# Optimization experiments

Hardware: AMD Instinct MI355X
Metric: run time of the kernel (lower is better)

Reference implementation:

```python
import jax, jax.numpy as jnp
import numpy as np

NT, NV, ND, NM, NP = 50000, 1000, 20000, 5000, 8000
E = 100000
D, H, C = 256, 4, 64          # gnn_hidden_dim, heads, per-head channels
TS_FEAT, EMB, L = 64, 128, 2
NEG_SLOPE = 0.2

SIZES = {'ts': NT, 'vital': NV, 'diag': ND, 'med': NM, 'proc': NP}
EDGE_TYPES = [('ts', 'vital'), ('vital', 'ts'), ('ts', 'diag'), ('diag', 'ts'),
              ('ts', 'med'), ('med', 'ts'), ('ts', 'proc'), ('proc', 'ts')]
T = len(EDGE_TYPES)


def setup_inputs():
    key = jax.random.key(0)
    ks = jax.random.split(key, 32)
    def nrm(k, shape, s=0.05):
        return jax.random.normal(k, shape, dtype=jnp.float32) * s
    inp = {}
    inp['ts_x'] = nrm(ks[0], (NT, TS_FEAT), 1.0)
    inp['emb_vital'] = nrm(ks[1], (NV, EMB), 1.0)
    inp['emb_diag'] = nrm(ks[2], (ND, EMB), 1.0)
    inp['emb_med'] = nrm(ks[3], (NM, EMB), 1.0)
    inp['emb_proc'] = nrm(ks[4], (NP, EMB), 1.0)
    inp['Wp_ts'] = nrm(ks[5], (TS_FEAT, D)); inp['bp_ts'] = jnp.zeros((D,), jnp.float32)
    inp['Wp_c'] = nrm(ks[6], (4, EMB, D)); inp['bp_c'] = jnp.zeros((4, D), jnp.float32)
    inp['Wsrc'] = nrm(ks[7], (L, T, D, H * C))
    inp['Wdst'] = nrm(ks[8], (L, T, D, H * C))
    inp['asrc'] = nrm(ks[9], (L, T, H, C))
    inp['adst'] = nrm(ks[10], (L, T, H, C))
    inp['bconv'] = jnp.zeros((L, T, H * C), jnp.float32)
    inp['Wc1'] = nrm(ks[11], (D, D // 2)); inp['bc1'] = jnp.zeros((D // 2,), jnp.float32)
    inp['Wc2'] = nrm(ks[12], (D // 2, 1)); inp['bc2'] = jnp.zeros((1,), jnp.float32)
    names = ['ei_tv', 'ei_vt', 'ei_td', 'ei_dt', 'ei_tm', 'ei_mt', 'ei_tp', 'ei_pt']
    for i, ((s, d), nm) in enumerate(zip(EDGE_TYPES, names)):
        k1, k2 = jax.random.split(ks[13 + i])
        src = jax.random.randint(k1, (E,), 0, SIZES[s], dtype=jnp.int32)
        dst = jax.random.randint(k2, (E,), 0, SIZES[d], dtype=jnp.int32)
        inp[nm] = jnp.stack([src, dst])
    return inp


def gat_conv(xs, xd, Ws, Wd, a_s, a_d, b, ei, nd):
    """Bipartite PyG GATConv: add_self_loops=False, concat heads, eval (no dropout)."""
    hs = (xs @ Ws).reshape(-1, H, C)            # [Ns,H,C]
    hd = (xd @ Wd).reshape(-1, H, C)            # [Nd,H,C]
    es = jnp.sum(hs * a_s, axis=-1)             # [Ns,H]
    ed = jnp.sum(hd * a_d, axis=-1)             # [Nd,H]
    src, dst = ei[0], ei[1]
    e = jax.nn.leaky_relu(es[src] + ed[dst], NEG_SLOPE)   # [E,H]
    m = jax.ops.segment_max(e, dst, num_segments=nd)      # segment softmax over dst
    ex = jnp.exp(e - m[dst])
    den = jax.ops.segment_sum(ex, dst, num_segments=nd)
    alpha = ex / (den[dst] + 1e-16)
    msg = (alpha[:, :, None] * hs[src]).reshape(-1, H * C)  # [E,H*C]
    return jax.ops.segment_sum(msg, dst, num_segments=nd) + b


def _forward(ts_x, emb_vital, emb_diag, emb_med, emb_proc, Wp_ts, bp_ts, Wp_c, bp_c,
             Wsrc, Wdst, asrc, adst, bconv, Wc1, bc1, Wc2, bc2, edges):
    x = {'ts': ts_x @ Wp_ts + bp_ts,
         'vital': emb_vital @ Wp_c[0] + bp_c[0],
         'diag': emb_diag @ Wp_c[1] + bp_c[1],
         'med': emb_med @ Wp_c[2] + bp_c[2],
         'proc': emb_proc @ Wp_c[3] + bp_c[3]}
    for l in range(L):
        new = {k: jnp.zeros((SIZES[k], D), jnp.float32) for k in x}  # HeteroConv aggr='sum'
        for t, ((s, d), ei) in enumerate(zip(EDGE_TYPES, edges)):
            new[d] = new[d] + gat_conv(x[s], x[d], Wsrc[l, t], Wdst[l, t],
                                       asrc[l, t], adst[l, t], bconv[l, t], ei, SIZES[d])
        x = {k: jax.nn.relu(v) for k, v in new.items()}
    g = jnp.mean(x['ts'], axis=0)               # graph embedding
    h = jax.nn.relu(g @ Wc1 + bc1)
    logits = h @ Wc2 + bc2
    return jnp.squeeze(logits, -1)              # output_classes == 1 -> scalar


def reference(ts_x, emb_vital, emb_diag, emb_med, emb_proc, Wp_ts, bp_ts, Wp_c, bp_c,
              Wsrc, Wdst, asrc, adst, bconv, Wc1, bc1, Wc2, bc2,
              ei_tv, ei_vt, ei_td, ei_dt, ei_tm, ei_mt, ei_tp, ei_pt):
    edges = (ei_tv, ei_vt, ei_td, ei_dt, ei_tm, ei_mt, ei_tp, ei_pt)
    return _forward(ts_x, emb_vital, emb_diag, emb_med, emb_proc, Wp_ts, bp_ts, Wp_c, bp_c,
                    Wsrc, Wdst, asrc, adst, bconv, Wc1, bc1, Wc2, bc2, edges)
```

## Files before the change

### kernel.cpp

```cpp
#include <hip/hip_runtime.h>

#define E_N 100000
#define NDST 234000

typedef __attribute__((ext_vector_type(8))) short bfrag8;
typedef __attribute__((ext_vector_type(4))) float accf4;

__device__ __forceinline__ void atomAddF(float* p, float v) { unsafeAtomicAdd(p, v); }
__device__ __forceinline__ float lrelu(float v) { return v >= 0.f ? v : 0.2f * v; }

__device__ __forceinline__ unsigned short f2bf(float f) {
    unsigned u = __float_as_uint(f);
    return (unsigned short)((u + 0x7FFFu + ((u >> 16) & 1u)) >> 16);
}
__device__ __forceinline__ float bf2f(unsigned short h) {
    return __uint_as_float(((unsigned)h) << 16);
}

__constant__ int c_tbase[8] = {0, 1000, 51000, 71000, 121000, 126000, 176000, 184000};
__constant__ int c_co4[4]   = {0, 1000, 21000, 26000};

struct EI8 { const int* p[8]; };

struct BTJob { const float* W; unsigned short* hi; unsigned short* lo; int K; int kshift; };
struct BTBatch { BTJob j[17]; };

struct MJob { const float* A; const unsigned short* BThi; const unsigned short* BTlo;
              float* C; unsigned short* Cbf; const float* bias; int M; int K; int relu; };
struct MBatch { MJob j[8]; };

__device__ __forceinline__ void gemm_body(const MJob jb, int bx)
{
    const int rowblk = (bx >> 4) * 8 + (bx & 7);
    const int half = (bx >> 3) & 1;
    const int bm = rowblk * 128;
    if (bm >= jb.M) return;
    const int bn = half * 128;
    const int M = jb.M, K = jb.K;

    __shared__ unsigned short Ah[128 * 40];
    __shared__ unsigned short Al[128 * 40];
    __shared__ unsigned short B1[128 * 40];
    __shared__ unsigned short B2[128 * 40];

    const int tid  = threadIdx.x;
    const int wv   = tid >> 6;
    const int lane = tid & 63;
    const int qr = wv >> 1, qc = wv & 1;
    const int lm = lane & 15;
    const int lq = lane >> 4;

    accf4 acc[4][4] = {};

    for (int k0 = 0; k0 < K; k0 += 32) {
#pragma unroll
        for (int it = 0; it < 4; ++it) {
            int slot = it * 256 + tid;
            int m  = slot >> 3;
            int kq = (slot & 7) << 2;
            float4 v = make_float4(0.f, 0.f, 0.f, 0.f);
            if (bm + m < M) v = *(const float4*)(jb.A + (size_t)(bm + m) * K + k0 + kq);
            int o = m * 40 + kq;
            unsigned short h0 = f2bf(v.x), h1 = f2bf(v.y), h2 = f2bf(v.z), h3 = f2bf(v.w);
            Ah[o + 0] = h0; Ah[o + 1] = h1; Ah[o + 2] = h2; Ah[o + 3] = h3;
            Al[o + 0] = f2bf(v.x - bf2f(h0));
            Al[o + 1] = f2bf(v.y - bf2f(h1));
            Al[o + 2] = f2bf(v.z - bf2f(h2));
            Al[o + 3] = f2bf(v.w - bf2f(h3));
        }
#pragma unroll
        for (int it = 0; it < 2; ++it) {
            int slot = it * 256 + tid;
            int n  = slot >> 2;
            int kq = (slot & 3) << 3;
            size_t go = (size_t)(bn + n) * K + k0 + kq;
            *(uint4*)&B1[n * 40 + kq] = *(const uint4*)(jb.BThi + go);
            *(uint4*)&B2[n * 40 + kq] = *(const uint4*)(jb.BTlo + go);
        }
        __syncthreads();

        bfrag8 ah[4], al[4], b1[4], b2[4];
#pragma unroll
        for (int t = 0; t < 4; ++t) {
            int am  = qr * 64 + t * 16 + lm;
            int bnn = qc * 64 + t * 16 + lm;
            ah[t] = *(const bfrag8*)&Ah[am * 40 + lq * 8];
            al[t] = *(const bfrag8*)&Al[am * 40 + lq * 8];
            b1[t] = *(const bfrag8*)&B1[bnn * 40 + lq * 8];
            b2[t] = *(const bfrag8*)&B2[bnn * 40 + lq * 8];
        }
#pragma unroll
        for (int mt = 0; mt < 4; ++mt)
#pragma unroll
            for (int nt = 0; nt < 4; ++nt) {
                acc[mt][nt] = __builtin_amdgcn_mfma_f32_16x16x32_bf16(ah[mt], b1[nt], acc[mt][nt], 0, 0, 0);
                acc[mt][nt] = __builtin_amdgcn_mfma_f32_16x16x32_bf16(al[mt], b1[nt], acc[mt][nt], 0, 0, 0);
                acc[mt][nt] = __builtin_amdgcn_mfma_f32_16x16x32_bf16(ah[mt], b2[nt], acc[mt][nt], 0, 0, 0);
            }
        __syncthreads();
    }

#pragma unroll
    for (int nt = 0; nt < 4; ++nt) {
        int col = bn + qc * 64 + nt * 16 + lm;
        float bv = jb.bias ? jb.bias[col] : 0.f;
#pragma unroll
        for (int mt = 0; mt < 4; ++mt) {
            int row0 = bm + qr * 64 + mt * 16 + lq * 4;
#pragma unroll
            for (int r = 0; r < 4; ++r) {
                int row = row0 + r;
                if (row < M) {
                    float o = acc[mt][nt][r] + bv;
                    if (jb.relu) o = fmaxf(o, 0.f);
                    if (jb.C)   jb.C[(size_t)row * 256 + col] = o;
                    if (jb.Cbf) jb.Cbf[(size_t)row * 256 + col] = f2bf(o);
                }
            }
        }
    }
}

struct Prep1 { BTBatch bt; const float* Wsrc; const float* Wdst; const float* asrc;
               const float* adst; float* weff; EI8 ei; int* cnt; };

__global__ __launch_bounds__(256) void prep1_k(Prep1 a)
{
    int bx = blockIdx.x;
    if (bx < 4352) {
        BTJob jb = a.bt.j[bx >> 8];
        int idx = (bx & 255) * 256 + threadIdx.x;
        if (idx >= (jb.K << 8)) return;
        int n = idx >> jb.kshift;
        int k = idx & (jb.K - 1);
        float w = jb.W[(size_t)k * 256 + n];
        unsigned short h = f2bf(w);
        jb.hi[idx] = h;
        jb.lo[idx] = f2bf(w - bf2f(h));
    } else if (bx < 4672) {
        int idx = (bx - 4352) * 256 + threadIdx.x;
        if (idx >= 81920) return;
        int col = idx & 31;
        int k   = (idx >> 5) & 255;
        int lnt = idx >> 13;
        int nt  = lnt % 5;
        int l   = lnt / 5;
        bool is_src; int t, h;
        if (nt == 0) {
            if (col < 16) { is_src = true;  t = (col >> 2) * 2;            h = col & 3; }
            else          { is_src = false; t = ((col - 16) >> 2) * 2 + 1; h = col & 3; }
        } else {
            if (col < 4)      { is_src = true;  t = 2 * nt - 1; h = col; }
            else if (col < 8) { is_src = false; t = 2 * nt - 2; h = col - 4; }
            else { a.weff[idx] = 0.f; return; }
        }
        const float* W = (is_src ? a.Wsrc : a.Wdst) + ((size_t)((l * 8 + t) * 256 + k)) * 256 + h * 64;
        const float* av = (is_src ? a.asrc : a.adst) + ((size_t)((l * 8 + t) * 4 + h)) * 64;
        float val = 0.f;
        for (int c = 0; c < 64; c++) val += W[c] * av[c];
        a.weff[idx] = val;
    } else {
        int g = (bx - 4672) * 256 + threadIdx.x;
        if (g >= 8 * E_N) return;
        int t = g / E_N;
        int i = g - t * E_N;
        int d = a.ei.p[t][E_N + i];
        atomicAdd(&a.cnt[c_tbase[t] + d], 1);
    }
}

__global__ __launch_bounds__(256) void prep2_k(const float* __restrict__ Wp_ts,
                                               const float* __restrict__ bp_ts,
                                               const float* __restrict__ Wp_c,
                                               const float* __restrict__ bp_c,
                                               const float* __restrict__ weff,
                                               float* __restrict__ effT, float* __restrict__ biasT,
                                               float* __restrict__ effC, float* __restrict__ biasC,
                                               const int* __restrict__ cnt,
                                               int* __restrict__ rowptr, int* __restrict__ bsum)
{
    if (blockIdx.x < 25) {
        int idx = blockIdx.x * 256 + threadIdx.x;
        if (idx < 2048) {
            int kk = idx >> 5, j = idx & 31;
            float s = 0.f;
            for (int k = 0; k < 256; k++) s += Wp_ts[kk * 256 + k] * weff[k * 32 + j];
            effT[idx] = s;
        } else if (idx < 2080) {
            int j = idx - 2048;
            float s = 0.f;
            for (int k = 0; k < 256; k++) s += bp_ts[k] * weff[k * 32 + j];
            biasT[j] = s;
        } else if (idx < 2080 + 4 * 1032) {
            int r = idx - 2080;
            int q = r / 1032; r -= q * 1032;
            const float* wq = weff + (q + 1) * 8192;
            if (r < 1024) {
                int kk = r >> 3, j = r & 7;
                float s = 0.f;
                for (int k = 0; k < 256; k++) s += Wp_c[(size_t)q * 32768 + kk * 256 + k] * wq[k * 32 + j];
                effC[(q * 128 + kk) * 8 + j] = s;
            } else {
                int j = r - 1024;
                float s = 0.f;
                for (int k = 0; k < 256; k++) s += bp_c[q * 256 + k] * wq[k * 32 + j];
                biasC[q * 8 + j] = s;
            }
        }
    } else {
        __shared__ int sd[256];
        int b = blockIdx.x - 25, t = threadIdx.x;
        int base = b * 1024 + t * 4;
        int v0 = 0, v1 = 0, v2 = 0, v3 = 0;
        if (base + 0 < NDST) v0 = cnt[base + 0];
        if (base + 1 < NDST) v1 = cnt[base + 1];
        if (base + 2 < NDST) v2 = cnt[base + 2];
        if (base + 3 < NDST) v3 = cnt[base + 3];
        int s = v0 + v1 + v2 + v3;
        sd[t] = s;
        __syncthreads();
        for (int off = 1; off < 256; off <<= 1) {
            int x = 0;
            if (t >= off) x = sd[t - off];
            __syncthreads();
            if (t >= off) sd[t] += x;
            __syncthreads();
        }
        int run = sd[t] - s;
        if (t == 255) bsum[b] = sd[255];
        if (base + 0 < NDST) rowptr[base + 0] = run;          run += v0;
        if (base + 1 < NDST) rowptr[base + 1] = run;          run += v1;
        if (base + 2 < NDST) rowptr[base + 2] = run;          run += v2;
        if (base + 3 < NDST) rowptr[base + 3] = run;
    }
}

__global__ __launch_bounds__(256) void scanB(int* __restrict__ bsum, int nb)
{
    __shared__ int sd[256];
    int t = threadIdx.x;
    int v = (t < nb) ? bsum[t] : 0;
    sd[t] = v;
    __syncthreads();
    for (int off = 1; off < 256; off <<= 1) {
        int x = 0;
        if (t >= off) x = sd[t - off];
        __syncthreads();
        if (t >= off) sd[t] += x;
        __syncthreads();
    }
    if (t < nb) bsum[t] = sd[t] - v;
}

struct Prep3 { int* rowptr; const int* bsum; int* cursor;
               const float* ts_x; const float* effT; const float* biasT; float* attnT;
               const float* e0; const float* e1; const float* e2; const float* e3;
               const float* effC; const float* biasC; float* attnC; };

__global__ __launch_bounds__(256) void prep3_k(Prep3 a)
{
    int bx = blockIdx.x;
    if (bx < 229) {
        int t = threadIdx.x;
        int off = a.bsum[bx];
        int base = bx * 1024 + t * 4;
#pragma unroll
        for (int j = 0; j < 4; j++) {
            int i = base + j;
            if (i < NDST) {
                int r = a.rowptr[i] + off;
                a.rowptr[i] = r;
                a.cursor[i] = r;
            }
        }
        if (bx == 0 && t == 0) a.rowptr[NDST] = 8 * E_N;
    } else if (bx < 425) {
        int n = (bx - 229) * 256 + threadIdx.x;
        if (n >= 50000) return;
        float acc[32];
#pragma unroll
        for (int j = 0; j < 32; j++) acc[j] = a.biasT[j];
        const float* xr = a.ts_x + (size_t)n * 64;
        for (int k = 0; k < 64; k += 4) {
            float4 xv = *(const float4*)(xr + k);
#pragma unroll
            for (int j = 0; j < 32; j++)
                acc[j] += xv.x * a.effT[(k + 0) * 32 + j] + xv.y * a.effT[(k + 1) * 32 + j]
                        + xv.z * a.effT[(k + 2) * 32 + j] + xv.w * a.effT[(k + 3) * 32 + j];
        }
#pragma unroll
        for (int j = 0; j < 32; j++) a.attnT[(size_t)n * 32 + j] = acc[j];
    } else {
        int m = (bx - 425) * 256 + threadIdx.x;
        if (m >= 34000) return;
        int q, loc;
        if (m < 1000)       { q = 0; loc = m; }
        else if (m < 21000) { q = 1; loc = m - 1000; }
        else if (m < 26000) { q = 2; loc = m - 21000; }
        else                { q = 3; loc = m - 26000; }
        const float* er = (q == 0 ? a.e0 : q == 1 ? a.e1 : q == 2 ? a.e2 : a.e3) + (size_t)loc * 128;
        const float* W = a.effC + q * 1024;
        float acc[8];
#pragma unroll
        for (int j = 0; j < 8; j++) acc[j] = a.biasC[q * 8 + j];
        for (int k = 0; k < 128; k += 4) {
            float4 xv = *(const float4*)(er + k);
#pragma unroll
            for (int j = 0; j < 8; j++)
                acc[j] += xv.x * W[(k + 0) * 8 + j] + xv.y * W[(k + 1) * 8 + j]
                        + xv.z * W[(k + 2) * 8 + j] + xv.w * W[(k + 3) * 8 + j];
        }
#pragma unroll
        for (int j = 0; j < 8; j++) a.attnC[(size_t)m * 8 + j] = acc[j];
    }
}

struct ProjPlace { MBatch mb; EI8 ei; int* cursor; int* ssrc; int* sdst; float* exf;
                   const float* attnT; const float* attnC; };

__global__ __launch_bounds__(256, 2) void projplace_k(ProjPlace a)
{
    if (blockIdx.x < 3920) {
        gemm_body(a.mb.j[blockIdx.x / 784], blockIdx.x % 784);
    } else {
        int g = (blockIdx.x - 3920) * 256 + threadIdx.x;
        if (g >= 8 * E_N) return;
        int t = g / E_N;
        int i = g - t * E_N;
        int d = a.ei.p[t][E_N + i];
        int s = a.ei.p[t][i];
        int pos = atomicAdd(&a.cursor[c_tbase[t] + d], 1);
        a.ssrc[pos] = s;
        a.sdst[pos] = d;
        int q = t >> 1;
        float4 ex;
        if ((t & 1) == 0) {
            int w = c_co4[q] + d;
            int soff = 4 * q;
            ex.x = __expf(lrelu(a.attnT[(size_t)s * 32 + soff + 0] + a.attnC[(size_t)w * 8 + 4]));
            ex.y = __expf(lrelu(a.attnT[(size_t)s * 32 + soff + 1] + a.attnC[(size_t)w * 8 + 5]));
            ex.z = __expf(lrelu(a.attnT[(size_t)s * 32 + soff + 2] + a.attnC[(size_t)w * 8 + 6]));
            ex.w = __expf(lrelu(a.attnT[(size_t)s * 32 + soff + 3] + a.attnC[(size_t)w * 8 + 7]));
        } else {
            int m = c_co4[q] + s;
            int doff = 16 + 4 * q;
            ex.x = __expf(lrelu(a.attnC[(size_t)m * 8 + 0] + a.attnT[(size_t)d * 32 + doff + 0]));
            ex.y = __expf(lrelu(a.attnC[(size_t)m * 8 + 1] + a.attnT[(size_t)d * 32 + doff + 1]));
            ex.z = __expf(lrelu(a.attnC[(size_t)m * 8 + 2] + a.attnT[(size_t)d * 32 + doff + 2]));
            ex.w = __expf(lrelu(a.attnC[(size_t)m * 8 + 3] + a.attnT[(size_t)d * 32 + doff + 3]));
        }
        *(float4*)(a.exf + (size_t)pos * 4) = ex;
    }
}

__device__ __forceinline__ float4 agg_core(const float* __restrict__ exf,
                                           const unsigned short* __restrict__ hscbf,
                                           const int* __restrict__ rowptr,
                                           const int* __restrict__ ssrc,
                                           const float* __restrict__ bconv_l,
                                           int d, int h, int ch)
{
    const int co4[4] = {0, 1000, 21000, 26000};
    const int tb4[4] = {1000, 71000, 126000, 184000};
    const int bo4[4] = {256, 768, 1280, 1792};
    float ax = 0.f, ay = 0.f, az = 0.f, aw = 0.f;
#pragma unroll
    for (int q = 0; q < 4; q++) {
        int r0 = rowptr[tb4[q] + d], r1 = rowptr[tb4[q] + d + 1];
        float den = 0.f, sx = 0.f, sy = 0.f, sz = 0.f, sw = 0.f;
        int e = r0;
        for (; e + 2 <= r1; e += 2) {
            int sA = ssrc[e], sB = ssrc[e + 1];
            float xA = exf[(size_t)e * 4 + h];
            float xB = exf[(size_t)(e + 1) * 4 + h];
            ushort4 rA = *(const ushort4*)(hscbf + (size_t)(co4[q] + sA) * 256 + ch);
            ushort4 rB = *(const ushort4*)(hscbf + (size_t)(co4[q] + sB) * 256 + ch);
            den += xA + xB;
            sx += xA * bf2f(rA.x) + xB * bf2f(rB.x);
            sy += xA * bf2f(rA.y) + xB * bf2f(rB.y);
            sz += xA * bf2f(rA.z) + xB * bf2f(rB.z);
            sw += xA * bf2f(rA.w) + xB * bf2f(rB.w);
        }
        if (e < r1) {
            int s = ssrc[e];
            float x = exf[(size_t)e * 4 + h];
            den += x;
            ushort4 hv = *(const ushort4*)(hscbf + (size_t)(co4[q] + s) * 256 + ch);
            sx += x * bf2f(hv.x); sy += x * bf2f(hv.y);
            sz += x * bf2f(hv.z); sw += x * bf2f(hv.w);
        }
        const float* b = bconv_l + bo4[q] + ch;
        float inv = 1.f / (den + 1e-16f);
        ax += b[0] + sx * inv; ay += b[1] + sy * inv;
        az += b[2] + sz * inv; aw += b[3] + sw * inv;
    }
    float4 o;
    o.x = fmaxf(ax, 0.f); o.y = fmaxf(ay, 0.f);
    o.z = fmaxf(az, 0.f); o.w = fmaxf(aw, 0.f);
    return o;
}

struct L1A { MBatch mb; const float* exf; const unsigned short* xtsbf;
             const int* rowptr; const int* ssrc; float* aggx; };

__global__ __launch_bounds__(256, 2) void l1a_k(L1A a)
{
    if (blockIdx.x < 1280) {
        gemm_body(a.mb.j[blockIdx.x / 320], blockIdx.x % 320);
        return;
    }
    int w = (blockIdx.x - 1280) * 4 + (threadIdx.x >> 6);
    int lane = threadIdx.x & 63;
    int h = lane >> 4;
    int ch = (h << 6) | ((lane & 15) << 2);
    int q, dloc;
    if (w < 1000)       { q = 0; dloc = w; }
    else if (w < 21000) { q = 1; dloc = w - 1000; }
    else if (w < 26000) { q = 2; dloc = w - 21000; }
    else                { q = 3; dloc = w - 26000; }
    const int csr4[4] = {0, 51000, 121000, 176000};
    int r0 = a.rowptr[csr4[q] + dloc], r1 = a.rowptr[csr4[q] + dloc + 1];
    float den = 0.f, sx = 0.f, sy = 0.f, sz = 0.f, sw = 0.f;
    int e = r0;
    for (; e + 4 <= r1; e += 4) {
        int sA = a.ssrc[e], sB = a.ssrc[e + 1], sC = a.ssrc[e + 2], sD = a.ssrc[e + 3];
        float xA = a.exf[(size_t)e * 4 + h];
        float xB = a.exf[(size_t)(e + 1) * 4 + h];
        float xC = a.exf[(size_t)(e + 2) * 4 + h];
        float xD = a.exf[(size_t)(e + 3) * 4 + h];
        ushort4 rA = *(const ushort4*)(a.xtsbf + (size_t)sA * 256 + ch);
        ushort4 rB = *(const ushort4*)(a.xtsbf + (size_t)sB * 256 + ch);
        ushort4 rC = *(const ushort4*)(a.xtsbf + (size_t)sC * 256 + ch);
        ushort4 rD = *(const ushort4*)(a.xtsbf + (size_t)sD * 256 + ch);
        den += (xA + xB) + (xC + xD);
        sx += xA * bf2f(rA.x) + xB * bf2f(rB.x) + xC * bf2f(rC.x) + xD * bf2f(rD.x);
        sy += xA * bf2f(rA.y) + xB * bf2f(rB.y) + xC * bf2f(rC.y) + xD * bf2f(rD.y);
        sz += xA * bf2f(rA.z) + xB * bf2f(rB.z) + xC * bf2f(rC.z) + xD * bf2f(rD.z);
        sw += xA * bf2f(rA.w) + xB * bf2f(rB.w) + xC * bf2f(rC.w) + xD * bf2f(rD.w);
    }
    for (; e < r1; e++) {
        int s = a.ssrc[e];
        float x = a.exf[(size_t)e * 4 + h];
        den += x;
        ushort4 rv = *(const ushort4*)(a.xtsbf + (size_t)s * 256 + ch);
        sx += x * bf2f(rv.x); sy += x * bf2f(rv.y);
        sz += x * bf2f(rv.z); sw += x * bf2f(rv.w);
    }
    float inv = 1.f / (den + 1e-16f);
    float4 o; o.x = sx * inv; o.y = sy * inv; o.z = sz * inv; o.w = sw * inv;
    *(float4*)(a.aggx + (size_t)w * 256 + ch) = o;
}

struct L1B { MBatch mb; float* attnT; const float* exf; const unsigned short* hscbf;
             const int* rowptr; const int* ssrc; const float* bconv_l; const float* weff2; };

__global__ __launch_bounds__(256, 2) void l1b_k(L1B a)
{
    if (blockIdx.x < 1280) {
        gemm_body(a.mb.j[blockIdx.x / 320], blockIdx.x % 320);
        return;
    }
    int bx = blockIdx.x - 1280;
    int wv = threadIdx.x >> 6;
    int d = bx * 4 + wv;
    int lane = threadIdx.x & 63;
    int h = lane >> 4;
    int ch = (h << 6) | ((lane & 15) << 2);
    float4 o = agg_core(a.exf, a.hscbf, a.rowptr, a.ssrc, a.bconv_l, d, h, ch);
    __shared__ float rowbuf[4][256];
    rowbuf[wv][ch + 0] = o.x; rowbuf[wv][ch + 1] = o.y;
    rowbuf[wv][ch + 2] = o.z; rowbuf[wv][ch + 3] = o.w;
    __syncthreads();
    int j = lane & 15, seg = lane >> 4;
    const float* rb = rowbuf[wv] + seg * 64;
    const float* w2 = a.weff2 + (seg * 64) * 32 + 16 + j;
    float s = 0.f;
#pragma unroll 8
    for (int c = 0; c < 64; c++) s += rb[c] * w2[c * 32];
    s += __shfl_xor(s, 16);
    s += __shfl_xor(s, 32);
    if (lane < 16) a.attnT[(size_t)d * 32 + 16 + lane] = s;
}

struct L2A { MBatch mb; const float* x1; const float* weff2; float* attnC; };

__global__ __launch_bounds__(256, 2) void l2a_k(L2A a)
{
    if (blockIdx.x < 1280) {
        gemm_body(a.mb.j[blockIdx.x / 320], blockIdx.x % 320);
        return;
    }
    int m = (blockIdx.x - 1280) * 256 + threadIdx.x;
    if (m >= 34000) return;
    int n = 50000 + m;
    int nt = (n < 51000) ? 1 : (n < 71000) ? 2 : (n < 76000) ? 3 : 4;
    const float* xrow = a.x1 + (size_t)n * 256;
    const float* W = a.weff2 + nt * 8192;
    float acc[8];
#pragma unroll
    for (int j = 0; j < 8; j++) acc[j] = 0.f;
    for (int k = 0; k < 256; k += 4) {
        const float4 xv = *(const float4*)(xrow + k);
#pragma unroll
        for (int j = 0; j < 8; j++)
            acc[j] += xv.x * W[(k + 0) * 32 + j] + xv.y * W[(k + 1) * 32 + j]
                    + xv.z * W[(k + 2) * 32 + j] + xv.w * W[(k + 3) * 32 + j];
    }
#pragma unroll
    for (int j = 0; j < 8; j++) a.attnC[(size_t)m * 8 + j] = acc[j];
}

__global__ __launch_bounds__(256) void bake_k(const int* __restrict__ ssrc,
                                              const int* __restrict__ sdst,
                                              const float* __restrict__ attnC,
                                              const float* __restrict__ attnT,
                                              float* __restrict__ exf)
{
    int i = blockIdx.x * 256 + threadIdx.x;
    if (i >= 400000) return;
    int tq = i / E_N;
    int i2 = i - tq * E_N;
    int e = (2 * tq + 1) * E_N + i2;
    int s = ssrc[e], d = sdst[e];
    int m = c_co4[tq] + s;
    int doff = 16 + 4 * tq;
    float4 ex;
    ex.x = __expf(lrelu(attnC[(size_t)m * 8 + 0] + attnT[(size_t)d * 32 + doff + 0]));
    ex.y = __expf(lrelu(attnC[(size_t)m * 8 + 1] + attnT[(size_t)d * 32 + doff + 1]));
    ex.z = __expf(lrelu(attnC[(size_t)m * 8 + 2] + attnT[(size_t)d * 32 + doff + 2]));
    ex.w = __expf(lrelu(attnC[(size_t)m * 8 + 3] + attnT[(size_t)d * 32 + doff + 3]));
    *(float4*)(exf + (size_t)e * 4) = ex;
}

__global__ __launch_bounds__(256) void pool_k(const float* __restrict__ exf,
                                              const unsigned short* __restrict__ hscbf,
                                              const int* __restrict__ rowptr,
                                              const int* __restrict__ ssrc,
                                              const float* __restrict__ bconv_l,
                                              float* __restrict__ part)
{
    int d = blockIdx.x * 4 + (threadIdx.x >> 6);
    int lane = threadIdx.x & 63;
    int h = lane >> 4;
    int ch = (h << 6) | ((lane & 15) << 2);
    float4 o = agg_core(exf, hscbf, rowptr, ssrc, bconv_l, d, h, ch);
    __shared__ float4 red4[256];
    red4[threadIdx.x] = o;
    __syncthreads();
    if (threadIdx.x < 64) {
        float4 a = red4[threadIdx.x], b = red4[threadIdx.x + 64];
        float4 c = red4[threadIdx.x + 128], dd = red4[threadIdx.x + 192];
        float4 s;
        s.x = (a.x + b.x) + (c.x + dd.x);
        s.y = (a.y + b.y) + (c.y + dd.y);
        s.z = (a.z + b.z) + (c.z + dd.z);
        s.w = (a.w + b.w) + (c.w + dd.w);
        int cch = ((threadIdx.x >> 4) << 6) | ((threadIdx.x & 15) << 2);
        *(float4*)(part + (size_t)blockIdx.x * 256 + cch) = s;
    }
}

__global__ __launch_bounds__(256) void colsum_part(const float* __restrict__ part,
                                                   float* __restrict__ gsum)
{
    int c = threadIdx.x;
    float s = 0.f;
    for (int r = blockIdx.x; r < 12500; r += gridDim.x) s += part[(size_t)r * 256 + c];
    atomAddF(gsum + c, s);
}

__global__ __launch_bounds__(128) void head_k(const float* __restrict__ gsum,
                                              const float* __restrict__ Wc1,
                                              const float* __restrict__ bc1,
                                              const float* __restrict__ Wc2,
                                              const float* __restrict__ bc2,
                                              float* __restrict__ out)
{
    __shared__ float g[256];
    __shared__ float red[128];
    int t = threadIdx.x;
    g[t] = gsum[t] * (1.f / 50000.f);
    g[t + 128] = gsum[t + 128] * (1.f / 50000.f);
    __syncthreads();
    float acc = bc1[t];
    for (int k = 0; k < 256; k++) acc += g[k] * Wc1[k * 128 + t];
    red[t] = fmaxf(acc, 0.f) * Wc2[t];
    __syncthreads();
    for (int sft = 64; sft > 0; sft >>= 1) {
        if (t < sft) red[t] += red[t + sft];
        __syncthreads();
    }
    if (t == 0) out[0] = red[0] + bc2[0];
}

extern "C" void kernel_launch(void* const* d_in, const int* in_sizes, int n_in,
                              void* d_out, int out_size, void* d_ws, size_t ws_size,
                              hipStream_t stream)
{
    const float* ts_x   = (const float*)d_in[0];
    const float* emb[4] = {(const float*)d_in[1], (const float*)d_in[2],
                           (const float*)d_in[3], (const float*)d_in[4]};
    const float* Wp_ts  = (const float*)d_in[5];
    const float* bp_ts  = (const float*)d_in[6];
    const float* Wp_c   = (const float*)d_in[7];
    const float* bp_c   = (const float*)d_in[8];
    const float* Wsrc   = (const float*)d_in[9];
    const float* Wdst   = (const float*)d_in[10];
    const float* asrc   = (const float*)d_in[11];
    const float* adst   = (const float*)d_in[12];
    const float* bconv  = (const float*)d_in[13];
    const float* Wc1    = (const float*)d_in[14];
    const float* bc1    = (const float*)d_in[15];
    const float* Wc2    = (const float*)d_in[16];
    const float* bc2    = (const float*)d_in[17];
    EI8 ei;
    for (int t = 0; t < 8; t++) ei.p[t] = (const int*)d_in[18 + t];

    float* x0    = (float*)d_ws;
    float* x1    = x0    + 21504000;
    float* attnT = x1    + 21504000;
    float* attnC = attnT + 1600000;
    float* weff  = attnC + 272000;
    float* gsum  = weff  + 81920;
    float* effT  = gsum  + 256;
    float* biasT = effT  + 2048;
    float* effC  = biasT + 32;
    float* biasC = effC  + 4096;
    int* rowptr  = (int*)(biasC + 32);
    int* bsum    = rowptr + 234004;
    int* ssrc    = bsum + 256;
    unsigned short* xtsbf = (unsigned short*)(ssrc + 800000);
    unsigned short* hscbf = xtsbf + 12800000;
    unsigned short* btp   = hscbf + 8704000;
    int* cursor  = (int*)hscbf;
    float* aggx  = x1;
    float* exf   = x0;
    int* sdst    = (int*)(x0 + 3200000);
    float* part  = x0 + 4200000;

    unsigned short* bt_ts_h = btp;
    unsigned short* bt_ts_l = bt_ts_h + 16384;
    unsigned short* bt_c_h[4], *bt_c_l[4];
    {
        unsigned short* p = bt_ts_l + 16384;
        for (int q = 0; q < 4; q++) { bt_c_h[q] = p; p += 32768; bt_c_l[q] = p; p += 32768; }
    }
    unsigned short* bt_w = bt_ts_l + 16384 + 8 * 32768;
    auto wpan_h = [&](int l, int t) { return bt_w + (size_t)((l == 0 ? t : 8 + t / 2) * 2) * 65536; };
    auto wpan_l = [&](int l, int t) { return wpan_h(l, t) + 65536; };

    static const int Nd4[4]    = {1000, 20000, 5000, 8000};
    static const int co4[4]    = {0, 1000, 21000, 26000};
    static const int dbase4[4] = {50000, 51000, 71000, 76000};
    static const int tsrc[4]   = {1, 3, 5, 7};
    static const int tdst[4]   = {0, 2, 4, 6};

    hipMemsetAsync(cursor, 0, NDST * sizeof(int), stream);

    {
        Prep1 a = {};
        int zi = 0;
        a.bt.j[zi++] = {Wp_ts, bt_ts_h, bt_ts_l, 64, 6};
        for (int q = 0; q < 4; q++)
            a.bt.j[zi++] = {Wp_c + q * 32768, bt_c_h[q], bt_c_l[q], 128, 7};
        for (int t = 0; t < 8; t++)
            a.bt.j[zi++] = {Wsrc + (size_t)(0 * 8 + t) * 65536, wpan_h(0, t), wpan_l(0, t), 256, 8};
        for (int t = 1; t < 8; t += 2)
            a.bt.j[zi++] = {Wsrc + (size_t)(1 * 8 + t) * 65536, wpan_h(1, t), wpan_l(1, t), 256, 8};
        a.Wsrc = Wsrc; a.Wdst = Wdst; a.asrc = asrc; a.adst = adst;
        a.weff = weff; a.ei = ei; a.cnt = cursor;
        prep1_k<<<7797, 256, 0, stream>>>(a);
    }

    prep2_k<<<254, 256, 0, stream>>>(Wp_ts, bp_ts, Wp_c, bp_c, weff,
                                     effT, biasT, effC, biasC, cursor, rowptr, bsum);
    scanB<<<1, 256, 0, stream>>>(bsum, 229);

    {
        Prep3 a = {rowptr, bsum, cursor, ts_x, effT, biasT, attnT,
                   emb[0], emb[1], emb[2], emb[3], effC, biasC, attnC};
        prep3_k<<<558, 256, 0, stream>>>(a);
    }

    {
        ProjPlace a = {};
        a.mb.j[0] = {ts_x, bt_ts_h, bt_ts_l, nullptr, xtsbf, bp_ts, 50000, 64, 0};
        for (int q = 0; q < 4; q++)
            a.mb.j[1 + q] = {emb[q], bt_c_h[q], bt_c_l[q], x0 + (size_t)dbase4[q] * 256,
                             nullptr, bp_c + q * 256, Nd4[q], 128, 0};
        a.ei = ei; a.cursor = cursor; a.ssrc = ssrc; a.sdst = sdst; a.exf = exf;
        a.attnT = attnT; a.attnC = attnC;
        projplace_k<<<7045, 256, 0, stream>>>(a);
    }

    {
        L1A a = {};
        for (int q = 0; q < 4; q++)
            a.mb.j[q] = {x0 + (size_t)dbase4[q] * 256, wpan_h(0, tsrc[q]), wpan_l(0, tsrc[q]),
                         nullptr, hscbf + (size_t)co4[q] * 256, nullptr, Nd4[q], 256, 0};
        a.exf = exf; a.xtsbf = xtsbf; a.rowptr = rowptr; a.ssrc = ssrc; a.aggx = aggx;
        l1a_k<<<9780, 256, 0, stream>>>(a);
    }

    {
        L1B a = {};
        for (int q = 0; q < 4; q++)
            a.mb.j[q] = {aggx + (size_t)co4[q] * 256, wpan_h(0, tdst[q]), wpan_l(0, tdst[q]),
                         x1 + (size_t)dbase4[q] * 256, nullptr, bconv + tdst[q] * 256, Nd4[q], 256, 1};
        a.attnT = attnT; a.exf = exf; a.hscbf = hscbf; a.rowptr = rowptr; a.ssrc = ssrc;
        a.bconv_l = bconv; a.weff2 = weff + 40960;
        l1b_k<<<13780, 256, 0, stream>>>(a);
    }

    {
        L2A a = {};
        for (int q = 0; q < 4; q++)
            a.mb.j[q] = {x1 + (size_t)dbase4[q] * 256, wpan_h(1, tsrc[q]), wpan_l(1, tsrc[q]),
                         nullptr, hscbf + (size_t)co4[q] * 256, nullptr, Nd4[q], 256, 0};
        a.x1 = x1; a.weff2 = weff + 40960; a.attnC = attnC;
        l2a_k<<<1413, 256, 0, stream>>>(a);
    }

    bake_k<<<1563, 256, 0, stream>>>(ssrc, sdst, attnC, attnT, exf);
    hipMemsetAsync(gsum, 0, 256 * sizeof(float), stream);
    pool_k<<<12500, 256, 0, stream>>>(exf, hscbf, rowptr, ssrc, bconv + 2048, part);
    colsum_part<<<256, 256, 0, stream>>>(part, gsum);
    head_k<<<1, 128, 0, stream>>>(gsum, Wc1, bc1, Wc2, bc2, (float*)d_out);
}
```

Baseline: 718.5 us.

## Split fused GEMM+aggregation kernels into aggregation, batched GEMM, and fold kernels

The two layer-1 kernels used to pair a 4-job GEMM with an edge aggregation pass in a single launch. They are now three launches: a standalone aggx aggregation, one 8-job batched GEMM covering both previous GEMM sets, and a standalone fold kernel. The aggregation and fold kernels drop the 2-blocks-per-SM launch bound, so the memory-bound gather code is no longer held to the GEMM's occupancy limits. The cost is losing the overlap of GEMM and gather work within one launch, plus an extra kernel launch. It also depends on MBatch holding at least 8 jobs, which the old code only filled to 4.

```diff
diff --git a/kernel.cpp b/kernel.cpp
--- a/kernel.cpp
+++ b/kernel.cpp
@@ -119,6 +119,11 @@
             }
         }
     }
+}
+
+__global__ __launch_bounds__(256, 2) void gemm_mb(MBatch b)
+{
+    gemm_body(b.j[blockIdx.x / 320], blockIdx.x % 320);
 }
 
 struct Prep1 { BTBatch bt; const float* Wsrc; const float* Wdst; const float* asrc;
@@ -400,16 +405,13 @@
     return o;
 }
 
-struct L1A { MBatch mb; const float* exf; const unsigned short* xtsbf;
-             const int* rowptr; const int* ssrc; float* aggx; };
-
-__global__ __launch_bounds__(256, 2) void l1a_k(L1A a)
-{
-    if (blockIdx.x < 1280) {
-        gemm_body(a.mb.j[blockIdx.x / 320], blockIdx.x % 320);
-        return;
-    }
-    int w = (blockIdx.x - 1280) * 4 + (threadIdx.x >> 6);
+__global__ __launch_bounds__(256) void aggx_k(const float* __restrict__ exf,
+                                              const unsigned short* __restrict__ xtsbf,
+                                              const int* __restrict__ rowptr,
+                                              const int* __restrict__ ssrc,
+                                              float* __restrict__ aggx)
+{
+    int w = blockIdx.x * 4 + (threadIdx.x >> 6);
     int lane = threadIdx.x & 63;
     int h = lane >> 4;
     int ch = (h << 6) | ((lane & 15) << 2);
@@ -419,19 +421,19 @@
     else if (w < 26000) { q = 2; dloc = w - 21000; }
     else                { q = 3; dloc = w - 26000; }
     const int csr4[4] = {0, 51000, 121000, 176000};
-    int r0 = a.rowptr[csr4[q] + dloc], r1 = a.rowptr[csr4[q] + dloc + 1];
+    int r0 = rowptr[csr4[q] + dloc], r1 = rowptr[csr4[q] + dloc + 1];
     float den = 0.f, sx = 0.f, sy = 0.f, sz = 0.f, sw = 0.f;
     int e = r0;
     for (; e + 4 <= r1; e += 4) {
-        int sA = a.ssrc[e], sB = a.ssrc[e + 1], sC = a.ssrc[e + 2], sD = a.ssrc[e + 3];
-        float xA = a.exf[(size_t)e * 4 + h];
-        float xB = a.exf[(size_t)(e + 1) * 4 + h];
-        float xC = a.exf[(size_t)(e + 2) * 4 + h];
-        float xD = a.exf[(size_t)(e + 3) * 4 + h];
-        ushort4 rA = *(const ushort4*)(a.xtsbf + (size_t)sA * 256 + ch);
-        ushort4 rB = *(const ushort4*)(a.xtsbf + (size_t)sB * 256 + ch);
-        ushort4 rC = *(const ushort4*)(a.xtsbf + (size_t)sC * 256 + ch);
-        ushort4 rD = *(const ushort4*)(a.xtsbf + (size_t)sD * 256 + ch);
+        int sA = ssrc[e], sB = ssrc[e + 1], sC = ssrc[e + 2], sD = ssrc[e + 3];
+        float xA = exf[(size_t)e * 4 + h];
+        float xB = exf[(size_t)(e + 1) * 4 + h];
+        float xC = exf[(size_t)(e + 2) * 4 + h];
+        float xD = exf[(size_t)(e + 3) * 4 + h];
+        ushort4 rA = *(const ushort4*)(xtsbf + (size_t)sA * 256 + ch);
+        ushort4 rB = *(const ushort4*)(xtsbf + (size_t)sB * 256 + ch);
+        ushort4 rC = *(const ushort4*)(xtsbf + (size_t)sC * 256 + ch);
+        ushort4 rD = *(const ushort4*)(xtsbf + (size_t)sD * 256 + ch);
         den += (xA + xB) + (xC + xD);
         sx += xA * bf2f(rA.x) + xB * bf2f(rB.x) + xC * bf2f(rC.x) + xD * bf2f(rD.x);
         sy += xA * bf2f(rA.y) + xB * bf2f(rB.y) + xC * bf2f(rC.y) + xD * bf2f(rD.y);
@@ -439,47 +441,45 @@
         sw += xA * bf2f(rA.w) + xB * bf2f(rB.w) + xC * bf2f(rC.w) + xD * bf2f(rD.w);
     }
     for (; e < r1; e++) {
-        int s = a.ssrc[e];
-        float x = a.exf[(size_t)e * 4 + h];
+        int s = ssrc[e];
+        float x = exf[(size_t)e * 4 + h];
         den += x;
-        ushort4 rv = *(const ushort4*)(a.xtsbf + (size_t)s * 256 + ch);
+        ushort4 rv = *(const ushort4*)(xtsbf + (size_t)s * 256 + ch);
         sx += x * bf2f(rv.x); sy += x * bf2f(rv.y);
         sz += x * bf2f(rv.z); sw += x * bf2f(rv.w);
     }
     float inv = 1.f / (den + 1e-16f);
     float4 o; o.x = sx * inv; o.y = sy * inv; o.z = sz * inv; o.w = sw * inv;
-    *(float4*)(a.aggx + (size_t)w * 256 + ch) = o;
-}
-
-struct L1B { MBatch mb; float* attnT; const float* exf; const unsigned short* hscbf;
-             const int* rowptr; const int* ssrc; const float* bconv_l; const float* weff2; };
-
-__global__ __launch_bounds__(256, 2) void l1b_k(L1B a)
-{
-    if (blockIdx.x < 1280) {
-        gemm_body(a.mb.j[blockIdx.x / 320], blockIdx.x % 320);
-        return;
-    }
-    int bx = blockIdx.x - 1280;
+    *(float4*)(aggx + (size_t)w * 256 + ch) = o;
+}
+
+__global__ __launch_bounds__(256) void fold_k(float* __restrict__ attnT,
+                                              const float* __restrict__ exf,
+                                              const unsigned short* __restrict__ hscbf,
+                                              const int* __restrict__ rowptr,
+                                              const int* __restrict__ ssrc,
+                                              const float* __restrict__ bconv_l,
+                                              const float* __restrict__ weff2)
+{
     int wv = threadIdx.x >> 6;
-    int d = bx * 4 + wv;
+    int d = blockIdx.x * 4 + wv;
     int lane = threadIdx.x & 63;
     int h = lane >> 4;
     int ch = (h << 6) | ((lane & 15) << 2);
-    float4 o = agg_core(a.exf, a.hscbf, a.rowptr, a.ssrc, a.bconv_l, d, h, ch);
+    float4 o = agg_core(exf, hscbf, rowptr, ssrc, bconv_l, d, h, ch);
     __shared__ float rowbuf[4][256];
     rowbuf[wv][ch + 0] = o.x; rowbuf[wv][ch + 1] = o.y;
     rowbuf[wv][ch + 2] = o.z; rowbuf[wv][ch + 3] = o.w;
     __syncthreads();
     int j = lane & 15, seg = lane >> 4;
     const float* rb = rowbuf[wv] + seg * 64;
-    const float* w2 = a.weff2 + (seg * 64) * 32 + 16 + j;
+    const float* w2 = weff2 + (seg * 64) * 32 + 16 + j;
     float s = 0.f;
 #pragma unroll 8
     for (int c = 0; c < 64; c++) s += rb[c] * w2[c * 32];
     s += __shfl_xor(s, 16);
     s += __shfl_xor(s, 32);
-    if (lane < 16) a.attnT[(size_t)d * 32 + 16 + lane] = s;
+    if (lane < 16) attnT[(size_t)d * 32 + 16 + lane] = s;
 }
 
 struct L2A { MBatch mb; const float* x1; const float* weff2; float* attnC; };
@@ -675,7 +675,6 @@
     prep2_k<<<254, 256, 0, stream>>>(Wp_ts, bp_ts, Wp_c, bp_c, weff,
                                      effT, biasT, effC, biasC, cursor, rowptr, bsum);
     scanB<<<1, 256, 0, stream>>>(bsum, 229);
-
     {
         Prep3 a = {rowptr, bsum, cursor, ts_x, effT, biasT, attnT,
                    emb[0], emb[1], emb[2], emb[3], effC, biasC, attnC};
@@ -693,24 +692,20 @@
         projplace_k<<<7045, 256, 0, stream>>>(a);
     }
 
+    aggx_k<<<8500, 256, 0, stream>>>(exf, xtsbf, rowptr, ssrc, aggx);
+
     {
-        L1A a = {};
+        MBatch b = {};
         for (int q = 0; q < 4; q++)
-            a.mb.j[q] = {x0 + (size_t)dbase4[q] * 256, wpan_h(0, tsrc[q]), wpan_l(0, tsrc[q]),
-                         nullptr, hscbf + (size_t)co4[q] * 256, nullptr, Nd4[q], 256, 0};
-        a.exf = exf; a.xtsbf = xtsbf; a.rowptr = rowptr; a.ssrc = ssrc; a.aggx = aggx;
-        l1a_k<<<9780, 256, 0, stream>>>(a);
-    }
-
-    {
-        L1B a = {};
+            b.j[q] = {x0 + (size_t)dbase4[q] * 256, wpan_h(0, tsrc[q]), wpan_l(0, tsrc[q]),
+                      nullptr, hscbf + (size_t)co4[q] * 256, nullptr, Nd4[q], 256, 0};
         for (int q = 0; q < 4; q++)
-            a.mb.j[q] = {aggx + (size_t)co4[q] * 256, wpan_h(0, tdst[q]), wpan_l(0, tdst[q]),
-                         x1 + (size_t)dbase4[q] * 256, nullptr, bconv + tdst[q] * 256, Nd4[q], 256, 1};
-        a.attnT = attnT; a.exf = exf; a.hscbf = hscbf; a.rowptr = rowptr; a.ssrc = ssrc;
-        a.bconv_l = bconv; a.weff2 = weff + 40960;
-        l1b_k<<<13780, 256, 0, stream>>>(a);
-    }
+            b.j[4 + q] = {aggx + (size_t)co4[q] * 256, wpan_h(0, tdst[q]), wpan_l(0, tdst[q]),
+                          x1 + (size_t)dbase4[q] * 256, nullptr, bconv + tdst[q] * 256, Nd4[q], 256, 1};
+        gemm_mb<<<2560, 256, 0, stream>>>(b);
+    }
+
+    fold_k<<<12500, 256, 0, stream>>>(attnT, exf, hscbf, rowptr, ssrc, bconv, weff + 40960);
 
     {
         L2A a = {};
```

After: 644.8 us. -10.3%, faster.
